# Kernel optimization log

Measured on AMD Instinct MI355X. Metric: run time of the kernel, lower is better.

The kernel has to match this reference:

```python
import jax, jax.numpy as jnp
import numpy as np

N = 100_000          # NEURON_COUNT (scaled)
INPUT_SIZE = 1024    # input neurons occupy indices [0, INPUT_SIZE)
OUTPUT_SIZE = 256    # output neurons occupy indices [N-OUTPUT_SIZE, N)
E = 10_000_000       # SYNAPSE_RATIO * N
STEPS = 3


def setup_inputs() -> dict:
    key = jax.random.key(0)
    k1, k2, k3, k4, k5 = jax.random.split(key, 5)
    x = jax.random.normal(k1, (INPUT_SIZE,), dtype=jnp.float32)
    synapse_weights = jax.random.normal(k2, (E,), dtype=jnp.float32)
    neuron_biases = jax.random.normal(k3, (N - INPUT_SIZE,), dtype=jnp.float32)
    synapse_src = jax.random.randint(k4, (E,), 0, N, dtype=jnp.int64) if jax.config.jax_enable_x64 else jax.random.randint(k4, (E,), 0, N, dtype=jnp.int32)
    synapse_dst = jax.random.randint(k5, (E,), 0, N, dtype=jnp.int64) if jax.config.jax_enable_x64 else jax.random.randint(k5, (E,), 0, N, dtype=jnp.int32)
    return {
        "x": x,
        "synapse_weights": synapse_weights,
        "neuron_biases": neuron_biases,
        "synapse_src": synapse_src,
        "synapse_dst": synapse_dst,
    }


def reference(x, synapse_weights, neuron_biases, synapse_src, synapse_dst):
    # Initial state: zeros everywhere, inputs injected at the first INPUT_SIZE slots.
    v = jnp.zeros((N,), dtype=x.dtype).at[:INPUT_SIZE].set(x.reshape(-1))
    # tanh applied to all neurons except outputs (last OUTPUT_SIZE indices)
    tanh_mask = jnp.arange(N) < (N - OUTPUT_SIZE)
    for _ in range(STEPS):
        # vectorized gather-multiply-scatter: next[to] += v[from] * w  (one segment_sum)
        msg = v[synapse_src] * synapse_weights                       # [E]
        nxt = jax.ops.segment_sum(msg, synapse_dst, num_segments=N)  # [N]
        # biases added to all non-input neurons
        nxt = nxt.at[INPUT_SIZE:].add(neuron_biases)
        # tanh everywhere except output neurons
        v = jnp.where(tanh_mask, jnp.tanh(nxt), nxt)
    return v[N - OUTPUT_SIZE:]
```

## Files before the change

### kernel.cpp

```cpp
#include <hip/hip_runtime.h>

#define N_NEURONS   100000
#define INPUT_SIZE  1024
#define OUTPUT_SIZE 256
#define E_SYN       10000000
#define STEPS       3

#define RANGES      8
#define BIN         12500
#define SCAT_BLK    512
#define CBLK        96
#define RG          8
#define RSL         (CBLK / RG)
#define CAP         1280000
#define RB_BLK      256
#define CH          4000
#define B_CNT       2500
#define VEC4        (E_SYN / 4)

__global__ void init_all(const float* __restrict__ x, float* __restrict__ v,
                         int* __restrict__ gcur) {
    int i = blockIdx.x * blockDim.x + threadIdx.x;
    if (i < N_NEURONS) v[i] = (i < INPUT_SIZE) ? x[i] : 0.0f;
    if (i < RANGES) gcur[i] = 0;
}

__global__ __launch_bounds__(RB_BLK) void reorder_partition(
        const float* __restrict__ w,
        const int*   __restrict__ src,
        const int*   __restrict__ dst,
        int2* __restrict__ recs,
        int*  __restrict__ gcur) {
    __shared__ int cnt[RANGES];
    __shared__ int cursor[RANGES];
    __shared__ int wbase[RB_BLK / 64][RANGES];
    const int tid  = threadIdx.x;
    const int lane = tid & 63;
    const int wv   = tid >> 6;
    const unsigned long long ltmask = (1ull << lane) - 1ull;
    if (tid < RANGES) cnt[tid] = 0;
    __syncthreads();

    const int beg  = blockIdx.x * CH;
    const int endx = beg + CH;
    const int ITER = (CH + RB_BLK - 1) / RB_BLK;
    const int* wi  = (const int*)w;

    int h[RANGES] = {0, 0, 0, 0, 0, 0, 0, 0};
    for (int it = 0; it < ITER; ++it) {
        int  e  = beg + it * RB_BLK + tid;
        bool ok = (e < endx);
        int  d  = ok ? dst[e] : 0;
        int  r  = d / BIN;
        unsigned long long okm = __ballot(ok);
        unsigned long long b0  = __ballot(r & 1);
        unsigned long long b1  = __ballot(r & 2);
        unsigned long long b2  = __ballot(r & 4);
#pragma unroll
        for (int rr = 0; rr < RANGES; ++rr) {
            unsigned long long m = ((rr & 1) ? b0 : ~b0) &
                                   ((rr & 2) ? b1 : ~b1) &
                                   ((rr & 4) ? b2 : ~b2) & okm;
            h[rr] += __popcll(m);
        }
    }
    if (lane < RANGES) {
        int t = h[0];
#pragma unroll
        for (int rr = 1; rr < RANGES; ++rr) if (lane == rr) t = h[rr];
        atomicAdd(&cnt[lane], t);
    }
    __syncthreads();
    if (tid < RANGES) cursor[tid] = tid * CAP + atomicAdd(&gcur[tid], cnt[tid]);
    __syncthreads();

    for (int it = 0; it < ITER; ++it) {
        int  e  = beg + it * RB_BLK + tid;
        bool ok = (e < endx);
        int  d  = ok ? dst[e] : 0;
        int  sv = ok ? src[e] : 0;
        int  wb = ok ? wi[e]  : 0;
        int  r  = d / BIN;
        unsigned long long okm = __ballot(ok);
        unsigned long long b0  = __ballot(r & 1);
        unsigned long long b1  = __ballot(r & 2);
        unsigned long long b2  = __ballot(r & 4);
        unsigned long long s0 = (lane & 1) ? b0 : ~b0;
        unsigned long long s1 = (lane & 2) ? b1 : ~b1;
        unsigned long long s2 = (lane & 4) ? b2 : ~b2;
        int tot = __popcll(s0 & s1 & s2 & okm);
        if (lane < RANGES) wbase[wv][lane] = atomicAdd(&cursor[lane], tot);
        unsigned long long m0 = (r & 1) ? b0 : ~b0;
        unsigned long long m1 = (r & 2) ? b1 : ~b1;
        unsigned long long m2 = (r & 4) ? b2 : ~b2;
        unsigned long long mym = m0 & m1 & m2 & okm;
        int base = wbase[wv][r];
        int pos  = base + __popcll(mym & ltmask);
        if (ok) recs[pos] = make_int2((sv << 14) | (d - r * BIN), wb);
    }
}

__global__ __launch_bounds__(SCAT_BLK) void scatter_sorted(
        const int2* __restrict__ recs,
        const int*  __restrict__ gcur,
        const float* __restrict__ v,
        float* __restrict__ partials) {
    __shared__ float bins[BIN];
    const int r = blockIdx.x / CBLK;
    const int c = blockIdx.x % CBLK;
    for (int j = threadIdx.x; j < BIN; j += SCAT_BLK) bins[j] = 0.0f;
    __syncthreads();

    const int cnt   = gcur[r];
    const int npair = cnt >> 1;
    const int4* base4 = (const int4*)(recs + (size_t)r * CAP);
    const int stride = CBLK * SCAT_BLK;
    int u = c * SCAT_BLK + threadIdx.x;
    for (; u + 3 * stride < npair; u += 4 * stride) {
        int4 a = base4[u];
        int4 b = base4[u + stride];
        int4 e = base4[u + 2 * stride];
        int4 f = base4[u + 3 * stride];
        float va0 = v[a.x >> 14];
        float va1 = v[a.z >> 14];
        float vb0 = v[b.x >> 14];
        float vb1 = v[b.z >> 14];
        float ve0 = v[e.x >> 14];
        float ve1 = v[e.z >> 14];
        float vf0 = v[f.x >> 14];
        float vf1 = v[f.z >> 14];
        atomicAdd(&bins[a.x & 16383], va0 * __int_as_float(a.y));
        atomicAdd(&bins[a.z & 16383], va1 * __int_as_float(a.w));
        atomicAdd(&bins[b.x & 16383], vb0 * __int_as_float(b.y));
        atomicAdd(&bins[b.z & 16383], vb1 * __int_as_float(b.w));
        atomicAdd(&bins[e.x & 16383], ve0 * __int_as_float(e.y));
        atomicAdd(&bins[e.z & 16383], ve1 * __int_as_float(e.w));
        atomicAdd(&bins[f.x & 16383], vf0 * __int_as_float(f.y));
        atomicAdd(&bins[f.z & 16383], vf1 * __int_as_float(f.w));
    }
    for (; u < npair; u += stride) {
        int4 a = base4[u];
        atomicAdd(&bins[a.x & 16383], v[a.x >> 14] * __int_as_float(a.y));
        atomicAdd(&bins[a.z & 16383], v[a.z >> 14] * __int_as_float(a.w));
    }
    if ((cnt & 1) && c == 0 && threadIdx.x == 0) {
        int2 p = recs[(size_t)r * CAP + cnt - 1];
        atomicAdd(&bins[p.x & 16383], v[p.x >> 14] * __int_as_float(p.y));
    }
    __syncthreads();
    float* o = partials + (size_t)(r * CBLK + c) * BIN;
    for (int j = threadIdx.x; j < BIN; j += SCAT_BLK) o[j] = bins[j];
}

__global__ void reduce_stage1(const float* __restrict__ partials,
                              float* __restrict__ p2) {
    int i4 = 4 * (blockIdx.x * blockDim.x + threadIdx.x);
    if (i4 >= N_NEURONS) return;
    const int g = blockIdx.y;
    const int r = i4 / BIN;
    const int j = i4 - r * BIN;
    const float* base = partials + ((size_t)(r * CBLK + g * RSL)) * BIN + j;
    float4 acc = {0.f, 0.f, 0.f, 0.f};
#pragma unroll
    for (int c = 0; c < RSL; ++c) {
        float4 p = *(const float4*)(base + (size_t)c * BIN);
        acc.x += p.x; acc.y += p.y; acc.z += p.z; acc.w += p.w;
    }
    *(float4*)(p2 + (size_t)g * N_NEURONS + i4) = acc;
}

__global__ void reduce_stage2(const float* __restrict__ p2,
                              const float* __restrict__ bias,
                              float* __restrict__ v,
                              float* __restrict__ out,
                              int write_out) {
    int i4 = 4 * (blockIdx.x * blockDim.x + threadIdx.x);
    if (i4 >= N_NEURONS) return;
    float4 acc = {0.f, 0.f, 0.f, 0.f};
#pragma unroll
    for (int g = 0; g < RG; ++g) {
        float4 p = *(const float4*)(p2 + (size_t)g * N_NEURONS + i4);
        acc.x += p.x; acc.y += p.y; acc.z += p.z; acc.w += p.w;
    }
    float av[4] = {acc.x, acc.y, acc.z, acc.w};
#pragma unroll
    for (int k = 0; k < 4; ++k) {
        int i = i4 + k;
        float val = av[k] + ((i >= INPUT_SIZE) ? bias[i - INPUT_SIZE] : 0.0f);
        float nv  = (i < N_NEURONS - OUTPUT_SIZE) ? tanhf(val) : val;
        v[i] = nv;
        if (write_out && i >= N_NEURONS - OUTPUT_SIZE)
            out[i - (N_NEURONS - OUTPUT_SIZE)] = val;
    }
}

__global__ void init_state_fb(const float* __restrict__ x, float* __restrict__ v) {
    int i = blockIdx.x * blockDim.x + threadIdx.x;
    if (i < N_NEURONS) v[i] = (i < INPUT_SIZE) ? x[i] : 0.0f;
}
__global__ void scatter_binned(const float* __restrict__ w,
                               const int*   __restrict__ src,
                               const int*   __restrict__ dst,
                               const float* __restrict__ v,
                               float*       __restrict__ partials,
                               int C) {
    __shared__ float bins[BIN];
    const int r = blockIdx.x / C;
    const int c = blockIdx.x % C;
    const int lo = r * BIN;
    const int hi = lo + BIN;
    for (int j = threadIdx.x; j < BIN; j += blockDim.x) bins[j] = 0.0f;
    __syncthreads();
    const int4*   src4 = (const int4*)src;
    const int4*   dst4 = (const int4*)dst;
    const float4* w4v  = (const float4*)w;
    const int stride = C * blockDim.x;
    for (int u = c * blockDim.x + threadIdx.x; u < VEC4; u += stride) {
        const int4   s4 = src4[u];
        const int4   d4 = dst4[u];
        const float4 wv = w4v[u];
        int   s[4] = {s4.x, s4.y, s4.z, s4.w};
        int   d[4] = {d4.x, d4.y, d4.z, d4.w};
        float ww[4] = {wv.x, wv.y, wv.z, wv.w};
#pragma unroll
        for (int k = 0; k < 4; ++k)
            if (d[k] >= lo && d[k] < hi)
                atomicAdd(&bins[d[k] - lo], v[s[k]] * ww[k]);
    }
    __syncthreads();
    float* o = partials + ((size_t)(r * C + c)) * BIN;
    for (int j = threadIdx.x; j < BIN; j += blockDim.x) o[j] = bins[j];
}
__global__ void reduce_update_fb(const float* __restrict__ partials,
                                 const float* __restrict__ bias,
                                 float* __restrict__ v,
                                 float* __restrict__ out,
                                 int C, int write_out) {
    int i4 = 4 * (blockIdx.x * blockDim.x + threadIdx.x);
    if (i4 >= N_NEURONS) return;
    const int r = i4 / BIN;
    const int j = i4 - r * BIN;
    const float* base = partials + ((size_t)r * C) * BIN + j;
    float4 acc = {0.f, 0.f, 0.f, 0.f};
    for (int c = 0; c < C; ++c) {
        float4 p = *(const float4*)(base + (size_t)c * BIN);
        acc.x += p.x; acc.y += p.y; acc.z += p.z; acc.w += p.w;
    }
    float av[4] = {acc.x, acc.y, acc.z, acc.w};
#pragma unroll
    for (int k = 0; k < 4; ++k) {
        int i = i4 + k;
        float val = av[k] + ((i >= INPUT_SIZE) ? bias[i - INPUT_SIZE] : 0.0f);
        float nv  = (i < N_NEURONS - OUTPUT_SIZE) ? tanhf(val) : val;
        v[i] = nv;
        if (write_out && i >= N_NEURONS - OUTPUT_SIZE)
            out[i - (N_NEURONS - OUTPUT_SIZE)] = val;
    }
}

extern "C" void kernel_launch(void* const* d_in, const int* in_sizes, int n_in,
                              void* d_out, int out_size, void* d_ws, size_t ws_size,
                              hipStream_t stream) {
    const float* x    = (const float*)d_in[0];
    const float* w    = (const float*)d_in[1];
    const float* bias = (const float*)d_in[2];
    const int*   src  = (const int*)d_in[3];
    const int*   dst  = (const int*)d_in[4];
    float* out = (float*)d_out;

    const int blk = 256;
    const int grid_n   = (N_NEURONS + blk - 1) / blk;
    const int red_grid = (N_NEURONS / 4 + blk - 1) / blk;

    float* v        = (float*)d_ws;
    float* partials = v + N_NEURONS;
    float* p2       = partials + (size_t)RANGES * CBLK * BIN;
    int2*  recs     = (int2*)(p2 + (size_t)RG * N_NEURONS);
    int*   gcur     = (int*)(recs + (size_t)RANGES * CAP);
    size_t need = (size_t)((char*)(gcur + RANGES) - (char*)d_ws);

    if (ws_size >= need) {
        init_all<<<grid_n, blk, 0, stream>>>(x, v, gcur);
        reorder_partition<<<B_CNT, RB_BLK, 0, stream>>>(w, src, dst, recs, gcur);
        for (int s = 0; s < STEPS; ++s) {
            scatter_sorted<<<RANGES * CBLK, SCAT_BLK, 0, stream>>>(
                recs, gcur, v, partials);
            reduce_stage1<<<dim3(red_grid, RG), blk, 0, stream>>>(partials, p2);
            reduce_stage2<<<red_grid, blk, 0, stream>>>(
                p2, bias, v, out, s == STEPS - 1 ? 1 : 0);
        }
    } else {
        long C = (long)(ws_size / 4 / N_NEURONS) - 1;
        if (C > 64) C = 64;
        if (C < 1) C = 1;
        float* part_fb = v + N_NEURONS;
        init_state_fb<<<grid_n, blk, 0, stream>>>(x, v);
        for (int s = 0; s < STEPS; ++s) {
            scatter_binned<<<RANGES * (int)C, SCAT_BLK, 0, stream>>>(
                w, src, dst, v, part_fb, (int)C);
            reduce_update_fb<<<red_grid, blk, 0, stream>>>(
                part_fb, bias, v, out, (int)C, s == STEPS - 1 ? 1 : 0);
        }
    }
}
```

Before: 421.4 us.

## Stage partitioned records in per-wave LDS ring buffers and flush coalesced 64-record chunks

Rewrites the reorder/partition kernel to load dst/src/weights as int4 vectors, process four edges per thread per iteration, and buffer each wave's records per destination range in a shared-memory ring buffer. Once 64 records accumulate for a range, the wave writes them as one contiguous, coalesced chunk to the global record array, replacing scattered per-element writes. Scatter block size and count and the chunk size are also retuned. The trade is extra LDS traffic, more shared memory per block and lower occupancy for more coalesced global stores.

Measured after the change: 398.4 us. 5.4% less time.

```diff
diff --git a/kernel.cpp b/kernel.cpp
--- a/kernel.cpp
+++ b/kernel.cpp
@@ -8,14 +8,16 @@
 
 #define RANGES      8
 #define BIN         12500
-#define SCAT_BLK    512
-#define CBLK        96
+#define SCAT_BLK    1024
+#define CBLK        64
 #define RG          8
 #define RSL         (CBLK / RG)
 #define CAP         1280000
 #define RB_BLK      256
-#define CH          4000
-#define B_CNT       2500
+#define RB_WAVES    4
+#define CH          8192
+#define B_CNT       1221
+#define STG_CAP     128
 #define VEC4        (E_SYN / 4)
 
 __global__ void init_all(const float* __restrict__ x, float* __restrict__ v,
@@ -32,8 +34,8 @@
         int2* __restrict__ recs,
         int*  __restrict__ gcur) {
     __shared__ int cnt[RANGES];
-    __shared__ int cursor[RANGES];
-    __shared__ int wbase[RB_BLK / 64][RANGES];
+    __shared__ int blk_cur[RANGES];
+    __shared__ int2 stg[RB_WAVES][RANGES][STG_CAP];
     const int tid  = threadIdx.x;
     const int lane = tid & 63;
     const int wv   = tid >> 6;
@@ -41,62 +43,109 @@
     if (tid < RANGES) cnt[tid] = 0;
     __syncthreads();
 
-    const int beg  = blockIdx.x * CH;
-    const int endx = beg + CH;
-    const int ITER = (CH + RB_BLK - 1) / RB_BLK;
-    const int* wi  = (const int*)w;
-
-    int h[RANGES] = {0, 0, 0, 0, 0, 0, 0, 0};
+    const long beg = (long)blockIdx.x * CH;
+    const int4* dst4 = (const int4*)dst;
+    const int4* src4 = (const int4*)src;
+    const int4* wq4  = (const int4*)w;
+    const int ITER = CH / (RB_BLK * 4);
+
+    {
+        int h[RANGES] = {0, 0, 0, 0, 0, 0, 0, 0};
+        for (int it = 0; it < ITER; ++it) {
+            long e  = beg + (long)it * RB_BLK * 4 + (long)tid * 4;
+            bool ok = (e < E_SYN);
+            int4 d4 = ok ? dst4[e >> 2] : make_int4(0, 0, 0, 0);
+            unsigned long long okm = __ballot(ok);
+            int rk[4] = {d4.x / BIN, d4.y / BIN, d4.z / BIN, d4.w / BIN};
+#pragma unroll
+            for (int k = 0; k < 4; ++k) {
+                unsigned long long b0 = __ballot(rk[k] & 1);
+                unsigned long long b1 = __ballot(rk[k] & 2);
+                unsigned long long b2 = __ballot(rk[k] & 4);
+#pragma unroll
+                for (int rr = 0; rr < RANGES; ++rr) {
+                    unsigned long long m = ((rr & 1) ? b0 : ~b0) &
+                                           ((rr & 2) ? b1 : ~b1) &
+                                           ((rr & 4) ? b2 : ~b2) & okm;
+                    h[rr] += __popcll(m);
+                }
+            }
+        }
+        if (lane < RANGES) {
+            int t = h[0];
+#pragma unroll
+            for (int rr = 1; rr < RANGES; ++rr) if (lane == rr) t = h[rr];
+            atomicAdd(&cnt[lane], t);
+        }
+    }
+    __syncthreads();
+    if (tid < RANGES) blk_cur[tid] = tid * CAP + atomicAdd(&gcur[tid], cnt[tid]);
+    __syncthreads();
+
+    int wr[RANGES] = {0, 0, 0, 0, 0, 0, 0, 0};
+    int fl[RANGES] = {0, 0, 0, 0, 0, 0, 0, 0};
     for (int it = 0; it < ITER; ++it) {
-        int  e  = beg + it * RB_BLK + tid;
-        bool ok = (e < endx);
-        int  d  = ok ? dst[e] : 0;
-        int  r  = d / BIN;
+        long e  = beg + (long)it * RB_BLK * 4 + (long)tid * 4;
+        bool ok = (e < E_SYN);
+        int4 d4 = ok ? dst4[e >> 2] : make_int4(0, 0, 0, 0);
+        int4 s4 = ok ? src4[e >> 2] : make_int4(0, 0, 0, 0);
+        int4 q4 = ok ? wq4[e >> 2]  : make_int4(0, 0, 0, 0);
         unsigned long long okm = __ballot(ok);
-        unsigned long long b0  = __ballot(r & 1);
-        unsigned long long b1  = __ballot(r & 2);
-        unsigned long long b2  = __ballot(r & 4);
-#pragma unroll
-        for (int rr = 0; rr < RANGES; ++rr) {
-            unsigned long long m = ((rr & 1) ? b0 : ~b0) &
-                                   ((rr & 2) ? b1 : ~b1) &
-                                   ((rr & 4) ? b2 : ~b2) & okm;
-            h[rr] += __popcll(m);
-        }
-    }
-    if (lane < RANGES) {
-        int t = h[0];
-#pragma unroll
-        for (int rr = 1; rr < RANGES; ++rr) if (lane == rr) t = h[rr];
-        atomicAdd(&cnt[lane], t);
-    }
-    __syncthreads();
-    if (tid < RANGES) cursor[tid] = tid * CAP + atomicAdd(&gcur[tid], cnt[tid]);
-    __syncthreads();
-
-    for (int it = 0; it < ITER; ++it) {
-        int  e  = beg + it * RB_BLK + tid;
-        bool ok = (e < endx);
-        int  d  = ok ? dst[e] : 0;
-        int  sv = ok ? src[e] : 0;
-        int  wb = ok ? wi[e]  : 0;
-        int  r  = d / BIN;
-        unsigned long long okm = __ballot(ok);
-        unsigned long long b0  = __ballot(r & 1);
-        unsigned long long b1  = __ballot(r & 2);
-        unsigned long long b2  = __ballot(r & 4);
-        unsigned long long s0 = (lane & 1) ? b0 : ~b0;
-        unsigned long long s1 = (lane & 2) ? b1 : ~b1;
-        unsigned long long s2 = (lane & 4) ? b2 : ~b2;
-        int tot = __popcll(s0 & s1 & s2 & okm);
-        if (lane < RANGES) wbase[wv][lane] = atomicAdd(&cursor[lane], tot);
-        unsigned long long m0 = (r & 1) ? b0 : ~b0;
-        unsigned long long m1 = (r & 2) ? b1 : ~b1;
-        unsigned long long m2 = (r & 4) ? b2 : ~b2;
-        unsigned long long mym = m0 & m1 & m2 & okm;
-        int base = wbase[wv][r];
-        int pos  = base + __popcll(mym & ltmask);
-        if (ok) recs[pos] = make_int2((sv << 14) | (d - r * BIN), wb);
+        int dd[4] = {d4.x, d4.y, d4.z, d4.w};
+        int ss[4] = {s4.x, s4.y, s4.z, s4.w};
+        int qq[4] = {q4.x, q4.y, q4.z, q4.w};
+#pragma unroll
+        for (int k = 0; k < 4; ++k) {
+            int r = dd[k] / BIN;
+            unsigned long long b0 = __ballot(r & 1);
+            unsigned long long b1 = __ballot(r & 2);
+            unsigned long long b2 = __ballot(r & 4);
+            unsigned long long mym = ((r & 1) ? b0 : ~b0) &
+                                     ((r & 2) ? b1 : ~b1) &
+                                     ((r & 4) ? b2 : ~b2) & okm;
+            int rank = __popcll(mym & ltmask);
+            int base = wr[0];
+            base = (r == 1) ? wr[1] : base;
+            base = (r == 2) ? wr[2] : base;
+            base = (r == 3) ? wr[3] : base;
+            base = (r == 4) ? wr[4] : base;
+            base = (r == 5) ? wr[5] : base;
+            base = (r == 6) ? wr[6] : base;
+            base = (r == 7) ? wr[7] : base;
+            int slot = (base + rank) & (STG_CAP - 1);
+            if (ok) stg[wv][r][slot] = make_int2((ss[k] << 14) | (dd[k] - r * BIN), qq[k]);
+#pragma unroll
+            for (int rr = 0; rr < RANGES; ++rr) {
+                unsigned long long m = ((rr & 1) ? b0 : ~b0) &
+                                       ((rr & 2) ? b1 : ~b1) &
+                                       ((rr & 4) ? b2 : ~b2) & okm;
+                wr[rr] += __popcll(m);
+            }
+#pragma unroll
+            for (int rr = 0; rr < RANGES; ++rr) {
+                if (wr[rr] - fl[rr] >= 64) {
+                    int gpos = 0;
+                    if (lane == 0) gpos = atomicAdd(&blk_cur[rr], 64);
+                    gpos = __shfl(gpos, 0, 64);
+                    int2 rec = stg[wv][rr][(fl[rr] & (STG_CAP - 1)) + lane];
+                    recs[(size_t)gpos + lane] = rec;
+                    fl[rr] += 64;
+                }
+            }
+        }
+    }
+#pragma unroll
+    for (int rr = 0; rr < RANGES; ++rr) {
+        int pend = wr[rr] - fl[rr];
+        if (pend > 0) {
+            int gpos = 0;
+            if (lane == 0) gpos = atomicAdd(&blk_cur[rr], pend);
+            gpos = __shfl(gpos, 0, 64);
+            if (lane < pend) {
+                int2 rec = stg[wv][rr][(fl[rr] & (STG_CAP - 1)) + lane];
+                recs[(size_t)gpos + lane] = rec;
+            }
+        }
     }
 }
 
```
